# Kernel tuning notes

Hardware: AMD Instinct MI355X
Metric: run time of the kernel (lower is better)

## Reference

```python
import jax, jax.numpy as jnp
import numpy as np
from jax import lax

B, N, C = 16, 16384, 90      # batch, anchors, classes
K = 100                      # per-class pre-NMS top-k
MAX_DET = 100                # final detections per image
IOU_THR = 0.5
SCORE_THR = 0.05


def setup_inputs() -> dict:
    key = jax.random.key(0)
    k1, k2, k3, k4 = jax.random.split(key, 4)
    box_encodings = jax.random.normal(k1, (B, N, 4), dtype=jnp.float32) * 0.5
    class_logits = jax.random.normal(k2, (B, N, C), dtype=jnp.float32) * 2.0 - 3.0
    # anchors as [ymin,xmin,ymax,xmax] in normalized coords
    centers = jax.random.uniform(k3, (N, 2), dtype=jnp.float32)             # (cy,cx)
    sizes = jax.random.uniform(k4, (N, 2), dtype=jnp.float32, minval=0.05, maxval=0.3)
    anchors = jnp.concatenate([centers - sizes / 2, centers + sizes / 2], axis=-1)
    return {"box_encodings": box_encodings, "class_logits": class_logits, "anchors": anchors}


def decode_boxes(enc, anchors):
    ymin, xmin, ymax, xmax = [anchors[:, i] for i in range(4)]
    ha, wa = ymax - ymin, xmax - xmin
    cya, cxa = (ymin + ymax) / 2, (xmin + xmax) / 2
    ty, tx, th, tw = enc[..., 0] / 10.0, enc[..., 1] / 10.0, enc[..., 2] / 5.0, enc[..., 3] / 5.0
    cy = ty * ha + cya
    cx = tx * wa + cxa
    h = jnp.exp(th) * ha
    w = jnp.exp(tw) * wa
    boxes = jnp.stack([cy - h / 2, cx - w / 2, cy + h / 2, cx + w / 2], axis=-1)
    return jnp.clip(boxes, 0.0, 1.0)  # [..., N, 4]


def pairwise_iou(b):  # b: [K,4]
    area = jnp.maximum(b[:, 2] - b[:, 0], 0) * jnp.maximum(b[:, 3] - b[:, 1], 0)
    iy = jnp.maximum(jnp.minimum(b[:, None, 2], b[None, :, 2]) - jnp.maximum(b[:, None, 0], b[None, :, 0]), 0)
    ix = jnp.maximum(jnp.minimum(b[:, None, 3], b[None, :, 3]) - jnp.maximum(b[:, None, 1], b[None, :, 1]), 0)
    inter = iy * ix
    union = area[:, None] + area[None, :] - inter
    return inter / jnp.maximum(union, 1e-8)


def nms_one_class(boxes, scores_c):  # boxes [N,4], scores_c [N]
    vals, idx = lax.top_k(scores_c, K)           # sorted descending
    bk = boxes[idx]                               # [K,4]
    iou = pairwise_iou(bk)                        # [K,K]
    def step(keep, i):
        supp = jnp.any(keep & (iou[i] >= IOU_THR))
        ki = (vals[i] > SCORE_THR) & (~supp)
        return keep.at[i].set(ki), None
    keep, _ = lax.scan(step, jnp.zeros((K,), bool), jnp.arange(K))
    return bk, vals * keep                        # suppressed -> score 0


def postprocess_one(boxes, scores):  # boxes [N,4], scores [N,C]
    bx_ck, sc_ck = jax.vmap(nms_one_class, in_axes=(None, 1))(boxes, scores)  # [C,K,4],[C,K]
    cls_ck = jnp.broadcast_to(jnp.arange(C, dtype=jnp.float32)[:, None], (C, K))
    sc_f = sc_ck.reshape(-1)
    fsc, fidx = lax.top_k(sc_f, MAX_DET)
    fbx = bx_ck.reshape(-1, 4)[fidx]
    fcl = cls_ck.reshape(-1)[fidx]
    return jnp.concatenate([fbx, fcl[:, None], fsc[:, None]], axis=-1)  # [MAX_DET, 6]


def reference(box_encodings, class_logits, anchors):
    boxes = decode_boxes(box_encodings, anchors)       # [B,N,4]
    scores = jax.nn.sigmoid(class_logits)              # [B,N,C]
    combined = jax.vmap(postprocess_one)(boxes, scores)  # [B,MAX_DET,6] = boxes|class|score
    return combined
```

## Files before the change

kernel.cpp:

```cpp
#include <hip/hip_runtime.h>
#include <stdint.h>
#include <math.h>

#define B_ 16
#define NN 16384
#define C_ 90
#define KSEL 100
#define MAXD 100
#define MFLAT (C_ * KSEL)
#define NPAIR 128


__device__ __forceinline__ uint32_t fkey(float f) {
  uint32_t u = __float_as_uint(f);
  return (u & 0x80000000u) ? ~u : (u | 0x80000000u);
}
__device__ __forceinline__ float keyinv(uint32_t k) {
  uint32_t u = (k & 0x80000000u) ? (k & 0x7FFFFFFFu) : ~k;
  return __uint_as_float(u);
}

__device__ __forceinline__ uint32_t blockSum512(uint32_t v, uint32_t* red, uint32_t* s_total) {
  int tid = threadIdx.x;
#pragma unroll
  for (int o = 32; o > 0; o >>= 1) v += __shfl_down(v, o, 64);
  if ((tid & 63) == 0) red[tid >> 6] = v;
  __syncthreads();
  if (tid == 0) {
    uint32_t s = 0;
#pragma unroll
    for (int i = 0; i < 8; ++i) s += red[i];
    *s_total = s;
  }
  __syncthreads();
  return *s_total;
}

__device__ __forceinline__ uint32_t blockSum256(uint32_t v, uint32_t* red, uint32_t* s_total) {
  int tid = threadIdx.x;
#pragma unroll
  for (int o = 32; o > 0; o >>= 1) v += __shfl_down(v, o, 64);
  if ((tid & 63) == 0) red[tid >> 6] = v;
  __syncthreads();
  if (tid == 0) *s_total = red[0] + red[1] + red[2] + red[3];
  __syncthreads();
  return *s_total;
}

__global__ __launch_bounds__(256) void transpose_key16_kernel(const float* __restrict__ logits,
                                                              uint16_t* __restrict__ keys16T) {
  __shared__ uint32_t tile[128 * 91];
  int b = blockIdx.y;
  int n0 = blockIdx.x * 128;
  const float4* src4 = reinterpret_cast<const float4*>(logits + ((size_t)b * NN + n0) * C_);
  for (int p = threadIdx.x; p < 2880; p += 256) {
    float4 v = src4[p];
    int e = p * 4;
    float vv[4] = {v.x, v.y, v.z, v.w};
#pragma unroll
    for (int j = 0; j < 4; ++j) {
      int ee = e + j;
      tile[(ee / C_) * 91 + (ee % C_)] = fkey(vv[j]);
    }
  }
  __syncthreads();
  uint16_t* dstb = keys16T + (size_t)b * C_ * NN + n0;
  for (int q = threadIdx.x; q < C_ * 16; q += 256) {
    int c = q >> 4, g = q & 15;
    int nn2 = g * 8;
    uint4 o;
    o.x = (tile[(nn2 + 0) * 91 + c] >> 16) | (tile[(nn2 + 1) * 91 + c] & 0xFFFF0000u);
    o.y = (tile[(nn2 + 2) * 91 + c] >> 16) | (tile[(nn2 + 3) * 91 + c] & 0xFFFF0000u);
    o.z = (tile[(nn2 + 4) * 91 + c] >> 16) | (tile[(nn2 + 5) * 91 + c] & 0xFFFF0000u);
    o.w = (tile[(nn2 + 6) * 91 + c] >> 16) | (tile[(nn2 + 7) * 91 + c] & 0xFFFF0000u);
    reinterpret_cast<uint4*>(dstb + (size_t)c * NN)[g] = o;
  }
}

template <int TR>
__global__ __launch_bounds__(512, 4) void select_kernel(
    const uint16_t* __restrict__ keys16T,
    const float* __restrict__ logits,
    uint32_t* __restrict__ candPacked,
    uint32_t* __restrict__ candCount) {
  __shared__ uint32_t hist[2048];
  __shared__ uint32_t sc[512];
  __shared__ uint32_t ws8[64];
  __shared__ int s_bsel;
  __shared__ uint32_t s_Sincl, s_Sexcl;
  __shared__ uint32_t red[8];
  __shared__ uint32_t s_total;
  __shared__ uint32_t s_cnt;

  const int c = blockIdx.x, b = blockIdx.y;
  const int tid = threadIdx.x;

  uint32_t keyw[16];
  if (TR) {
    const uint4* src4 = reinterpret_cast<const uint4*>(keys16T + ((size_t)b * C_ + c) * NN);
#pragma unroll
    for (int q = 0; q < 4; ++q) {
      uint4 kv = src4[q * 512 + tid];
      keyw[4 * q + 0] = kv.x; keyw[4 * q + 1] = kv.y;
      keyw[4 * q + 2] = kv.z; keyw[4 * q + 3] = kv.w;
    }
  } else {
    const float* src = logits + (size_t)b * NN * C_ + c;
#pragma unroll
    for (int m = 0; m < 16; ++m) {
      uint32_t i0 = (uint32_t)((((m >> 2) * 512 + tid) * 8) + ((m & 3) * 2));
      uint32_t klo = fkey(src[(size_t)i0 * C_]) >> 16;
      uint32_t khi = fkey(src[(size_t)(i0 + 1) * C_]) >> 16;
      keyw[m] = klo | (khi << 16);
    }
  }

  reinterpret_cast<uint4*>(hist)[tid] = make_uint4(0u, 0u, 0u, 0u);
  __syncthreads();
#pragma unroll
  for (int m = 0; m < 16; ++m) {
    uint32_t w = keyw[m];
    atomicAdd(&hist[(w & 0xFFFFu) >> 5], 1u);
    atomicAdd(&hist[w >> 21], 1u);
  }
  __syncthreads();

  uint32_t m_above = 0;
  uint32_t need = 100u;
  uint32_t cut16 = 0;
  int found = 0;
  int tiepath = 0;
  uint32_t V16 = 0, Texact = NN - 1;

  {
    uint32_t h0 = hist[4 * tid], h1 = hist[4 * tid + 1];
    uint32_t h2 = hist[4 * tid + 2], h3 = hist[4 * tid + 3];
    sc[tid] = h0 + h1 + h2 + h3;
    if (tid == 0) s_bsel = -1;
    __syncthreads();
    if (tid < 64) {
      uint32_t w = 0;
      int base = tid * 8;
#pragma unroll
      for (int i = 0; i < 8; ++i) w += sc[base + i];
#pragma unroll
      for (int off = 1; off < 64; off <<= 1) {
        uint32_t v = __shfl_down(w, off, 64);
        if (tid + off < 64) w += v;
      }
      ws8[tid] = w;
    }
    __syncthreads();
    {
      int g = tid >> 3;
      uint32_t above = (g < 63) ? ws8[g + 1] : 0u;
      for (int j = (g << 3) + 7; j > tid; --j) above += sc[j];
      uint32_t run = above;
      int best = -1;
      uint32_t bi = 0, be = 0;
      uint32_t hh[4] = {h0, h1, h2, h3};
#pragma unroll
      for (int p = 3; p >= 0; --p) {
        uint32_t h = hh[p];
        run += h;
        if (best < 0 && run >= need) { best = 4 * tid + p; bi = run; be = run - h; }
      }
      if (best >= 0) atomicMax(&s_bsel, best);
      __syncthreads();
      if (best >= 0 && best == s_bsel) { s_Sincl = bi; s_Sexcl = be; }
    }
    __syncthreads();

    uint32_t bsel = (uint32_t)s_bsel;
    uint32_t Sincl = s_Sincl, Sexcl = s_Sexcl;
    if (Sincl <= (uint32_t)NPAIR) {
      cut16 = bsel << 5;
      found = 1;
    } else {
      m_above = Sexcl;
      need = 100u - m_above;
      __syncthreads();
      if (tid < 8) reinterpret_cast<uint4*>(hist)[tid] = make_uint4(0u, 0u, 0u, 0u);
      __syncthreads();
#pragma unroll
      for (int m = 0; m < 16; ++m) {
        uint32_t w = keyw[m];
        uint32_t klo = w & 0xFFFFu, khi = w >> 16;
        if ((klo >> 5) == bsel) atomicAdd(&hist[klo & 31u], 1u);
        if ((khi >> 5) == bsel) atomicAdd(&hist[khi & 31u], 1u);
      }
      __syncthreads();
      uint32_t run = 0;
      int b1 = -1;
      uint32_t Si = 0, Se = 0;
      for (int p = 31; p >= 0; --p) {
        uint32_t h = hist[p];
        run += h;
        if (b1 < 0 && run >= need) { b1 = p; Si = run; Se = run - h; }
      }
      uint32_t cutv = (bsel << 5) | (uint32_t)b1;
      if (m_above + Si <= (uint32_t)NPAIR) {
        cut16 = cutv;
        found = 1;
      } else {
        tiepath = 1;
        V16 = cutv;
        m_above += Se;
        uint32_t r = 100u - m_above;
        uint32_t lo2 = 0, hi2 = NN - 1;
        while (lo2 < hi2) {
          uint32_t mid2 = lo2 + ((hi2 - lo2) >> 1);
          uint32_t cnt = 0;
#pragma unroll
          for (int m = 0; m < 16; ++m) {
            uint32_t w = keyw[m];
            uint32_t i0 = (uint32_t)((((m >> 2) * 512 + tid) * 8) + ((m & 3) * 2));
            cnt += ((w & 0xFFFFu) == V16 && i0 <= mid2) ? 1u : 0u;
            cnt += ((w >> 16) == V16 && (i0 + 1) <= mid2) ? 1u : 0u;
          }
          uint32_t tot = blockSum512(cnt, red, &s_total);
          if (tot >= r) hi2 = mid2; else lo2 = mid2 + 1;
        }
        Texact = lo2;
      }
    }
  }

  if (tid == 0) s_cnt = 0;
  __syncthreads();
  uint32_t* outp = candPacked + (size_t)(b * C_ + c) * NPAIR;
#pragma unroll
  for (int m = 0; m < 16; ++m) {
    uint32_t w = keyw[m];
    uint32_t i0 = (uint32_t)((((m >> 2) * 512 + tid) * 8) + ((m & 3) * 2));
    uint32_t klo = w & 0xFFFFu, khi = w >> 16;
    bool t0 = tiepath ? (klo > V16 || (klo == V16 && i0 <= Texact)) : (klo >= cut16);
    bool t1 = tiepath ? (khi > V16 || (khi == V16 && (i0 + 1) <= Texact)) : (khi >= cut16);
    if (t0) {
      uint32_t p = atomicAdd(&s_cnt, 1u);
      if (p < (uint32_t)NPAIR) outp[p] = (klo << 16) | i0;
    }
    if (t1) {
      uint32_t p = atomicAdd(&s_cnt, 1u);
      if (p < (uint32_t)NPAIR) outp[p] = (khi << 16) | (i0 + 1);
    }
  }
  __syncthreads();
  if (tid == 0) candCount[b * C_ + c] = (s_cnt > (uint32_t)NPAIR) ? (uint32_t)NPAIR : s_cnt;
}

__global__ __launch_bounds__(128, 4) void sort_nms_kernel(
    const uint32_t* __restrict__ candPacked,
    const uint32_t* __restrict__ candCount,
    const float* __restrict__ logits,
    const float* __restrict__ enc,
    const float* __restrict__ anchors,
    float* __restrict__ candBox,
    float* __restrict__ candScore) {
  __shared__ unsigned long long ck[NPAIR];
  __shared__ float s_vals[KSEL];
  __shared__ float s_boxv[KSEL][5];
  __shared__ float s_area[KSEL];
  __shared__ uint32_t smask[KSEL][4];
  __shared__ unsigned long long s_keepw[2];

  const int c = blockIdx.x, b = blockIdx.y;
  const int tid = threadIdx.x;
  const int bc = b * C_ + c;

  uint32_t cnt = candCount[bc];
  unsigned long long ckv = 0ull;
  if (tid < (int)cnt) {
    uint32_t v = candPacked[(size_t)bc * NPAIR + tid];
    int n = (int)(v & 0x3FFFu);
    float x = logits[((size_t)b * NN + n) * C_ + c];
    float s = 1.0f / (1.0f + expf(-x));
    ckv = ((unsigned long long)fkey(s) << 32) | (unsigned long long)(~(uint32_t)n);
  }
  ck[tid] = ckv;
  __syncthreads();

  for (int kk = 2; kk <= 128; kk <<= 1) {
    for (int j = kk >> 1; j > 0; j >>= 1) {
      int ixj = tid ^ j;
      if (ixj > tid) {
        unsigned long long a = ck[tid], bb2 = ck[ixj];
        if ((a < bb2) == ((tid & kk) == 0)) { ck[tid] = bb2; ck[ixj] = a; }
      }
      __syncthreads();
    }
  }

  if (tid < KSEL) {
    unsigned long long keyv = ck[tid];
    uint32_t hk = (uint32_t)(keyv >> 32);
    int n = (int)(~(uint32_t)(keyv & 0xFFFFFFFFull)) & (NN - 1);
    s_vals[tid] = keyinv(hk);
    float4 e = reinterpret_cast<const float4*>(enc)[(size_t)b * NN + n];
    float4 a = reinterpret_cast<const float4*>(anchors)[n];
    float ha = a.z - a.x, wa = a.w - a.y;
    float cya = (a.x + a.z) * 0.5f, cxa = (a.y + a.w) * 0.5f;
    float cy = (e.x / 10.0f) * ha + cya;
    float cx = (e.y / 10.0f) * wa + cxa;
    float h = expf(e.z / 5.0f) * ha;
    float w = expf(e.w / 5.0f) * wa;
    float y1 = fminf(fmaxf(cy - h * 0.5f, 0.0f), 1.0f);
    float x1 = fminf(fmaxf(cx - w * 0.5f, 0.0f), 1.0f);
    float y2 = fminf(fmaxf(cy + h * 0.5f, 0.0f), 1.0f);
    float x2 = fminf(fmaxf(cx + w * 0.5f, 0.0f), 1.0f);
    s_boxv[tid][0] = y1; s_boxv[tid][1] = x1; s_boxv[tid][2] = y2; s_boxv[tid][3] = x2;
    s_area[tid] = fmaxf(y2 - y1, 0.0f) * fmaxf(x2 - x1, 0.0f);
    smask[tid][0] = 0; smask[tid][1] = 0; smask[tid][2] = 0; smask[tid][3] = 0;
  }
  __syncthreads();

  for (int p = tid; p < (KSEL * (KSEL - 1)) / 2; p += 128) {
    int j = (int)((1.0f + sqrtf(1.0f + 8.0f * (float)p)) * 0.5f);
    while (j * (j - 1) / 2 > p) --j;
    while ((j + 1) * j / 2 <= p) ++j;
    int i = p - j * (j - 1) / 2;
    float iy1 = s_boxv[i][0], ix1 = s_boxv[i][1], iy2 = s_boxv[i][2], ix2 = s_boxv[i][3];
    float jy1 = s_boxv[j][0], jx1 = s_boxv[j][1], jy2 = s_boxv[j][2], jx2 = s_boxv[j][3];
    float ta = fmaxf(fminf(iy2, jy2) - fmaxf(iy1, jy1), 0.0f) *
               fmaxf(fminf(ix2, jx2) - fmaxf(ix1, jx1), 0.0f);
    float un = fmaxf(s_area[i] + s_area[j] - ta, 1e-8f);
    if (ta / un >= 0.5f) atomicOr(&smask[i][j >> 5], 1u << (j & 31));
  }
  __syncthreads();

  if (tid < 64) {
    int L = tid;
    unsigned long long r0 = (unsigned long long)smask[L][0] |
                            ((unsigned long long)smask[L][1] << 32);
    unsigned long long r1 = (unsigned long long)smask[L][2] |
                            ((unsigned long long)smask[L][3] << 32);
    unsigned long long r2 = 0, r3 = 0;
    if (L < KSEL - 64) {
      r2 = (unsigned long long)smask[L + 64][0] | ((unsigned long long)smask[L + 64][1] << 32);
      r3 = (unsigned long long)smask[L + 64][2] | ((unsigned long long)smask[L + 64][3] << 32);
    }
    unsigned long long vm0 = __ballot(s_vals[L] > 0.05f);
    unsigned long long vm1 = __ballot((L + 64 < KSEL) ? (s_vals[L + 64] > 0.05f) : false);
    unsigned long long supp0 = 0, supp1 = 0, k0 = 0, k1 = 0;
    for (int j = 0; j < KSEL; ++j) {
      unsigned long long rl, rh;
      bool pass;
      if (j < 64) {
        rl = __shfl(r0, j); rh = __shfl(r1, j);
        pass = ((vm0 >> j) & 1ull) && !((supp0 >> j) & 1ull);
      } else {
        rl = __shfl(r2, j - 64); rh = __shfl(r3, j - 64);
        pass = ((vm1 >> (j - 64)) & 1ull) && !((supp1 >> (j - 64)) & 1ull);
      }
      if (pass) {
        supp0 |= rl; supp1 |= rh;
        if (j < 64) k0 |= 1ull << j; else k1 |= 1ull << (j - 64);
      }
    }
    if (tid == 0) { s_keepw[0] = k0; s_keepw[1] = k1; }
  }
  __syncthreads();

  if (tid < KSEL) {
    bool kept = (tid < 64) ? ((s_keepw[0] >> tid) & 1ull)
                           : ((s_keepw[1] >> (tid - 64)) & 1ull);
    size_t base = (size_t)bc * KSEL + tid;
    candScore[base] = kept ? s_vals[tid] : 0.0f;
    float* cb = candBox + base * 4;
    cb[0] = s_boxv[tid][0]; cb[1] = s_boxv[tid][1];
    cb[2] = s_boxv[tid][2]; cb[3] = s_boxv[tid][3];
  }
}

#define FSLOT 36
__global__ __launch_bounds__(256, 4) void final_topk_kernel(
    const float* __restrict__ candScore,
    const float* __restrict__ candBox,
    float* __restrict__ out) {
  __shared__ uint32_t red[4];
  __shared__ uint32_t s_total;
  __shared__ uint32_t s_cnt;
  __shared__ unsigned long long ck[128];

  int b = blockIdx.x, tid = threadIdx.x;
  const float* src = candScore + (size_t)b * MFLAT;

  uint32_t key[FSLOT];
#pragma unroll
  for (int q = 0; q < FSLOT; ++q) {
    int idx = q * 256 + tid;
    key[q] = (idx < MFLAT) ? fkey(src[idx]) : 0u;
  }

  uint32_t lo = 0u, hi = 0xFFFFFFFFu;
  while (lo < hi) {
    uint32_t mid = lo + ((hi - lo) >> 1);
    uint32_t cnt = 0;
#pragma unroll
    for (int q = 0; q < FSLOT; ++q) cnt += (key[q] > mid) ? 1u : 0u;
    uint32_t tot = blockSum256(cnt, red, &s_total);
    if (tot >= (uint32_t)MAXD) lo = mid + 1; else hi = mid;
  }
  uint32_t V = lo;

  uint32_t cm = 0, ce = 0;
#pragma unroll
  for (int q = 0; q < FSLOT; ++q) {
    cm += (key[q] > V) ? 1u : 0u;
    ce += (key[q] == V) ? 1u : 0u;
  }
  uint32_t m = blockSum256(cm, red, &s_total);
  uint32_t t = blockSum256(ce, red, &s_total);
  uint32_t r = (uint32_t)MAXD - m;
  uint32_t T = (uint32_t)(MFLAT - 1);
  if (t != r) {
    uint32_t lo2 = 0, hi2 = (uint32_t)(MFLAT - 1);
    while (lo2 < hi2) {
      uint32_t mid2 = lo2 + ((hi2 - lo2) >> 1);
      uint32_t cnt = 0;
#pragma unroll
      for (int q = 0; q < FSLOT; ++q) {
        uint32_t idx = (uint32_t)(q * 256 + tid);
        cnt += (key[q] == V && idx <= mid2) ? 1u : 0u;
      }
      uint32_t tot = blockSum256(cnt, red, &s_total);
      if (tot >= r) hi2 = mid2; else lo2 = mid2 + 1;
    }
    T = lo2;
  }

  if (tid == 0) s_cnt = 0;
  __syncthreads();
#pragma unroll
  for (int q = 0; q < FSLOT; ++q) {
    uint32_t k = key[q];
    uint32_t idx = (uint32_t)(q * 256 + tid);
    if (k > V || (k == V && idx <= T)) {
      uint32_t p = atomicAdd(&s_cnt, 1u);
      if (p < 128u)
        ck[p] = ((unsigned long long)k << 32) | (unsigned long long)(~idx);
    }
  }
  __syncthreads();
  if (tid >= MAXD && tid < 128) ck[tid] = 0ull;
  __syncthreads();
  for (int kk = 2; kk <= 128; kk <<= 1) {
    for (int j = kk >> 1; j > 0; j >>= 1) {
      if (tid < 128) {
        int ixj = tid ^ j;
        if (ixj > tid) {
          unsigned long long a = ck[tid], bb = ck[ixj];
          if ((a < bb) == ((tid & kk) == 0)) { ck[tid] = bb; ck[ixj] = a; }
        }
      }
      __syncthreads();
    }
  }

  if (tid < MAXD) {
    unsigned long long keyv = ck[tid];
    int f = (int)(~(uint32_t)(keyv & 0xFFFFFFFFull));
    int c = f / KSEL;
    float sc = keyinv((uint32_t)(keyv >> 32));
    const float* cb = candBox + ((size_t)b * MFLAT + f) * 4;
    float* o = out + ((size_t)b * MAXD + tid) * 6;
    o[0] = cb[0]; o[1] = cb[1]; o[2] = cb[2]; o[3] = cb[3];
    o[4] = (float)c; o[5] = sc;
  }
}

extern "C" void kernel_launch(void* const* d_in, const int* in_sizes, int n_in,
                              void* d_out, int out_size, void* d_ws, size_t ws_size,
                              hipStream_t stream) {
  const float* enc = (const float*)d_in[0];
  const float* logits = (const float*)d_in[1];
  const float* anchors = (const float*)d_in[2];
  float* out = (float*)d_out;
  char* ws = (char*)d_ws;

  size_t off = 0;
  float* candBox = (float*)(ws + off);   off += (size_t)B_ * C_ * KSEL * 4 * sizeof(float);
  float* candScore = (float*)(ws + off); off += (size_t)B_ * C_ * KSEL * sizeof(float);
  uint32_t* candPacked = (uint32_t*)(ws + off);
  off += (size_t)B_ * C_ * NPAIR * sizeof(uint32_t);
  uint32_t* candCount = (uint32_t*)(ws + off); off += (size_t)B_ * C_ * sizeof(uint32_t);
  off = (off + 255) & ~(size_t)255;
  uint16_t* keys16T = (uint16_t*)(ws + off);
  size_t needT = off + (size_t)B_ * C_ * NN * sizeof(uint16_t);
  int transposed = (ws_size >= needT) ? 1 : 0;

  if (transposed) {
    transpose_key16_kernel<<<dim3(NN / 128, B_), 256, 0, stream>>>(logits, keys16T);
    select_kernel<1><<<dim3(C_, B_), 512, 0, stream>>>(keys16T, logits, candPacked, candCount);
  } else {
    select_kernel<0><<<dim3(C_, B_), 512, 0, stream>>>(keys16T, logits, candPacked, candCount);
  }

  sort_nms_kernel<<<dim3(C_, B_), 128, 0, stream>>>(candPacked, candCount, logits,
                                                    enc, anchors, candBox, candScore);

  final_topk_kernel<<<B_, 256, 0, stream>>>(candScore, candBox, out);
}
```

Before: 151.4 us.

## Replace binary-search threshold with 3-level radix histogram select in final top-k

The final top-k kernel previously found the 100th-largest key by a 32-step binary search, with a block-wide reduction at every step. It now builds up to three shared-memory histograms over 11/11/10-bit digits, using prefix scans to pick the bucket. It stops early once the candidate set fits in 128 slots, and the bitonic sort then orders the survivors. This cuts the number of block-wide synchronizations, at the cost of shared-memory atomics and a 2048-entry histogram that may lower occupancy.

```diff
diff --git a/kernel.cpp b/kernel.cpp
--- a/kernel.cpp
+++ b/kernel.cpp
@@ -377,6 +377,11 @@
     const float* __restrict__ candScore,
     const float* __restrict__ candBox,
     float* __restrict__ out) {
+  __shared__ uint32_t hist[2048];
+  __shared__ uint32_t sc[256];
+  __shared__ uint32_t ws4[64];
+  __shared__ int s_bsel;
+  __shared__ uint32_t s_Sincl, s_Sexcl;
   __shared__ uint32_t red[4];
   __shared__ uint32_t s_total;
   __shared__ uint32_t s_cnt;
@@ -392,28 +397,76 @@
     key[q] = (idx < MFLAT) ? fkey(src[idx]) : 0u;
   }
 
-  uint32_t lo = 0u, hi = 0xFFFFFFFFu;
-  while (lo < hi) {
-    uint32_t mid = lo + ((hi - lo) >> 1);
-    uint32_t cnt = 0;
-#pragma unroll
-    for (int q = 0; q < FSLOT; ++q) cnt += (key[q] > mid) ? 1u : 0u;
-    uint32_t tot = blockSum256(cnt, red, &s_total);
-    if (tot >= (uint32_t)MAXD) lo = mid + 1; else hi = mid;
-  }
-  uint32_t V = lo;
-
-  uint32_t cm = 0, ce = 0;
-#pragma unroll
-  for (int q = 0; q < FSLOT; ++q) {
-    cm += (key[q] > V) ? 1u : 0u;
-    ce += (key[q] == V) ? 1u : 0u;
-  }
-  uint32_t m = blockSum256(cm, red, &s_total);
-  uint32_t t = blockSum256(ce, red, &s_total);
-  uint32_t r = (uint32_t)MAXD - m;
-  uint32_t T = (uint32_t)(MFLAT - 1);
-  if (t != r) {
+  uint32_t cutHi = 0, m_above = 0, cut32 = 0;
+  int found = 0, tiepath = 0;
+  uint32_t V32 = 0, Texact = (uint32_t)(MFLAT - 1);
+
+  for (int lvl = 0; lvl < 3; ++lvl) {
+    const int shiftLo = (lvl == 0) ? 21 : (lvl == 1) ? 10 : 0;
+    const uint32_t mask = (lvl == 2) ? 0x3FFu : 0x7FFu;
+    const int nbits = (lvl == 2) ? 10 : 11;
+
+    for (int i = tid; i < 512; i += 256)
+      reinterpret_cast<uint4*>(hist)[i] = make_uint4(0u, 0u, 0u, 0u);
+    __syncthreads();
+#pragma unroll
+    for (int q = 0; q < FSLOT; ++q) {
+      uint32_t k = key[q];
+      bool in = (lvl == 0) ? true : ((k >> (shiftLo + nbits)) == cutHi);
+      if (in) atomicAdd(&hist[(k >> shiftLo) & mask], 1u);
+    }
+    __syncthreads();
+
+    const uint32_t need = 100u - m_above;
+
+    uint32_t h[8];
+#pragma unroll
+    for (int i = 0; i < 8; ++i) h[i] = hist[8 * tid + i];
+    sc[tid] = h[0] + h[1] + h[2] + h[3] + h[4] + h[5] + h[6] + h[7];
+    if (tid == 0) s_bsel = -1;
+    __syncthreads();
+    if (tid < 64) {
+      uint32_t w = sc[4 * tid] + sc[4 * tid + 1] + sc[4 * tid + 2] + sc[4 * tid + 3];
+#pragma unroll
+      for (int off = 1; off < 64; off <<= 1) {
+        uint32_t v = __shfl_down(w, off, 64);
+        if (tid + off < 64) w += v;
+      }
+      ws4[tid] = w;
+    }
+    __syncthreads();
+    {
+      int g = tid >> 2;
+      uint32_t above = (g < 63) ? ws4[g + 1] : 0u;
+      for (int j = (g << 2) + 3; j > tid; --j) above += sc[j];
+      uint32_t run = above;
+      int best = -1;
+      uint32_t bi = 0, be = 0;
+#pragma unroll
+      for (int p = 7; p >= 0; --p) {
+        run += h[p];
+        if (best < 0 && run >= need) { best = 8 * tid + p; bi = run; be = run - h[p]; }
+      }
+      if (best >= 0) atomicMax(&s_bsel, best);
+      __syncthreads();
+      if (best >= 0 && best == s_bsel) { s_Sincl = bi; s_Sexcl = be; }
+    }
+    __syncthreads();
+
+    uint32_t bsel = (uint32_t)s_bsel;
+    cutHi = (cutHi << nbits) | bsel;
+    if (m_above + s_Sincl <= 128u) {
+      cut32 = cutHi << shiftLo;
+      found = 1;
+      break;
+    }
+    m_above += s_Sexcl;
+  }
+
+  if (!found) {
+    tiepath = 1;
+    V32 = cutHi;
+    uint32_t r = 100u - m_above;
     uint32_t lo2 = 0, hi2 = (uint32_t)(MFLAT - 1);
     while (lo2 < hi2) {
       uint32_t mid2 = lo2 + ((hi2 - lo2) >> 1);
@@ -421,12 +474,12 @@
 #pragma unroll
       for (int q = 0; q < FSLOT; ++q) {
         uint32_t idx = (uint32_t)(q * 256 + tid);
-        cnt += (key[q] == V && idx <= mid2) ? 1u : 0u;
+        cnt += (key[q] == V32 && idx <= mid2) ? 1u : 0u;
       }
       uint32_t tot = blockSum256(cnt, red, &s_total);
       if (tot >= r) hi2 = mid2; else lo2 = mid2 + 1;
     }
-    T = lo2;
+    Texact = lo2;
   }
 
   if (tid == 0) s_cnt = 0;
@@ -435,15 +488,17 @@
   for (int q = 0; q < FSLOT; ++q) {
     uint32_t k = key[q];
     uint32_t idx = (uint32_t)(q * 256 + tid);
-    if (k > V || (k == V && idx <= T)) {
+    bool take = tiepath ? (k > V32 || (k == V32 && idx <= Texact)) : (k >= cut32);
+    if (take) {
       uint32_t p = atomicAdd(&s_cnt, 1u);
       if (p < 128u)
         ck[p] = ((unsigned long long)k << 32) | (unsigned long long)(~idx);
     }
   }
   __syncthreads();
-  if (tid >= MAXD && tid < 128) ck[tid] = 0ull;
-  __syncthreads();
+  if (tid < 128 && (uint32_t)tid >= s_cnt) ck[tid] = 0ull;
+  __syncthreads();
+
   for (int kk = 2; kk <= 128; kk <<= 1) {
     for (int j = kk >> 1; j > 0; j >>= 1) {
       if (tid < 128) {
@@ -461,11 +516,11 @@
     unsigned long long keyv = ck[tid];
     int f = (int)(~(uint32_t)(keyv & 0xFFFFFFFFull));
     int c = f / KSEL;
-    float sc = keyinv((uint32_t)(keyv >> 32));
+    float sc2 = keyinv((uint32_t)(keyv >> 32));
     const float* cb = candBox + ((size_t)b * MFLAT + f) * 4;
     float* o = out + ((size_t)b * MAXD + tid) * 6;
     o[0] = cb[0]; o[1] = cb[1]; o[2] = cb[2]; o[3] = cb[3];
-    o[4] = (float)c; o[5] = sc;
+    o[4] = (float)c; o[5] = sc2;
   }
 }
 
```

New measurement: 134.5 us. -11.2%, faster.
